# Kernel tuning notes

Measured on AMD Instinct MI355X. Metric: run time of the kernel, lower is better.

The kernel has to match this reference:

```python
import jax, jax.numpy as jnp
import numpy as np

D_MODEL = 1024
NUM_HEADS = 16
D_LATENT = 256
HEAD_DIM = D_MODEL // NUM_HEADS
BATCH = 2048
SEQ = 32


def setup_inputs() -> dict:
    key = jax.random.key(0)
    ks = jax.random.split(key, 9)
    s = 1.0 / np.sqrt(D_MODEL)
    sl = 1.0 / np.sqrt(D_LATENT)
    return {
        "x": jax.random.normal(ks[0], (BATCH, SEQ, D_MODEL), dtype=jnp.float32),
        "memory": jax.random.normal(ks[1], (BATCH, SEQ, D_LATENT), dtype=jnp.float32),
        "W_q": jax.random.normal(ks[2], (D_MODEL, D_MODEL), dtype=jnp.float32) * s,
        "W_k": jax.random.normal(ks[3], (D_MODEL, D_MODEL), dtype=jnp.float32) * s,
        "W_v": jax.random.normal(ks[4], (D_MODEL, D_MODEL), dtype=jnp.float32) * s,
        "W_o": jax.random.normal(ks[5], (D_MODEL, D_MODEL), dtype=jnp.float32) * s,
        "W_down_kv": jax.random.normal(ks[6], (D_MODEL, D_LATENT), dtype=jnp.float32) * s,
        "W_up_k": jax.random.normal(ks[7], (D_LATENT, D_MODEL), dtype=jnp.float32) * sl,
        "W_up_v": jax.random.normal(ks[8], (D_LATENT, D_MODEL), dtype=jnp.float32) * sl,
    }


def reference(x, memory, W_q, W_k, W_v, W_o, W_down_kv, W_up_k, W_up_v):
    B, S, _ = x.shape
    q = x @ W_q                     # [B,S,D]
    k = x @ W_k
    v = x @ W_v
    latent_kv = (k + v) @ W_down_kv  # [B,S,L]
    latent_kv = jnp.nan_to_num((latent_kv + memory) * 0.5)
    k_rec = latent_kv @ W_up_k       # [B,S,D]
    v_rec = latent_kv @ W_up_v
    # split heads: [B,H,S,hd]
    qh = q.reshape(B, S, NUM_HEADS, HEAD_DIM).transpose(0, 2, 1, 3)
    kh = k_rec.reshape(B, S, NUM_HEADS, HEAD_DIM).transpose(0, 2, 1, 3)
    vh = v_rec.reshape(B, S, NUM_HEADS, HEAD_DIM).transpose(0, 2, 1, 3)
    # NOTE: faithful to source — scale is sqrt(d_model), not sqrt(head_dim)
    scores = jnp.einsum("bhqd,bhkd->bhqk", qh, kh) / jnp.sqrt(jnp.float32(D_MODEL))
    scores = jnp.nan_to_num(scores, nan=0.0, posinf=10.0, neginf=-10.0)
    attn = jax.nn.softmax(scores, axis=-1)
    ctx = jnp.einsum("bhqk,bhkd->bhqd", attn, vh)
    ctx = ctx.transpose(0, 2, 1, 3).reshape(B, S, D_MODEL)
    out = ctx @ W_o
    return out, latent_kv
```

## Files before the change

kernel.cpp:

```cpp
#include <hip/hip_runtime.h>
#include <hip/hip_bf16.h>

typedef unsigned short u16;
typedef unsigned int u32;
typedef __attribute__((ext_vector_type(8))) __bf16 bf16x8;
typedef __attribute__((ext_vector_type(8))) unsigned short u16x8;
typedef __attribute__((ext_vector_type(4))) float floatx4;
typedef __attribute__((ext_vector_type(16))) float floatx16;

#define AS1 __attribute__((address_space(1)))
#define AS3 __attribute__((address_space(3)))

__device__ __forceinline__ u16 f2bf(float f) {
  unsigned u = __float_as_uint(f);
  u += 0x7fffu + ((u >> 16) & 1u);
  return (u16)(u >> 16);
}

__device__ __forceinline__ void g2lds16(const u16* g, u16* l) {
  __builtin_amdgcn_global_load_lds((AS1 void*)g, (AS3 void*)l, 16, 0, 0);
}

__device__ __forceinline__ void tcvt_body(const float* __restrict__ s,
                                          u16* __restrict__ d, int R, int C,
                                          int bx, int by, int tid,
                                          float (*t)[33]) {
  const int lx = tid & 31, ly = tid >> 5;
  const int x0 = bx * 32, y0 = by * 32;
  #pragma unroll
  for (int i = 0; i < 32; i += 8)
    t[ly + i][lx] = s[(size_t)(y0 + ly + i) * C + x0 + lx];
  __syncthreads();
  #pragma unroll
  for (int i = 0; i < 32; i += 8)
    d[(size_t)(x0 + ly + i) * R + y0 + lx] = f2bf(t[lx][ly + i]);
}

__global__ __launch_bounds__(256) void k_prep(
    const float* __restrict__ x, u16* __restrict__ Xb,
    const float* __restrict__ Wk, const float* __restrict__ Wv, u16* __restrict__ Wkv,
    const float* __restrict__ Wq, u16* __restrict__ WAt,
    const float* __restrict__ Wdn, u16* __restrict__ Wdt,
    const float* __restrict__ Wuk, u16* __restrict__ WBt,
    const float* __restrict__ Wuv, u16* __restrict__ WBt2,
    const float* __restrict__ Wo, u16* __restrict__ Wot) {
  __shared__ float t[32][33];
  const int b = blockIdx.x;
  const int tid = threadIdx.x;
  if (b < 4096) {
    long i = ((long)b * 256 + tid) * 8;
    const long stride = (long)4096 * 256 * 8;
    for (; i < 67108864L; i += stride) {
      float4 a = *(const float4*)(x + i);
      float4 c = *(const float4*)(x + i + 4);
      u16x8 o;
      o[0] = f2bf(a.x); o[1] = f2bf(a.y); o[2] = f2bf(a.z); o[3] = f2bf(a.w);
      o[4] = f2bf(c.x); o[5] = f2bf(c.y); o[6] = f2bf(c.z); o[7] = f2bf(c.w);
      *(u16x8*)(Xb + i) = o;
    }
  } else if (b < 4608) {
    long i = ((long)(b - 4096) * 256 + tid) * 8;
    float4 a0 = *(const float4*)(Wk + i);
    float4 a1 = *(const float4*)(Wk + i + 4);
    float4 b0 = *(const float4*)(Wv + i);
    float4 b1 = *(const float4*)(Wv + i + 4);
    u16x8 o;
    o[0] = f2bf(a0.x + b0.x); o[1] = f2bf(a0.y + b0.y);
    o[2] = f2bf(a0.z + b0.z); o[3] = f2bf(a0.w + b0.w);
    o[4] = f2bf(a1.x + b1.x); o[5] = f2bf(a1.y + b1.y);
    o[6] = f2bf(a1.z + b1.z); o[7] = f2bf(a1.w + b1.w);
    *(u16x8*)(Wkv + i) = o;
  } else if (b < 5632) {
    int lb = b - 4608;
    tcvt_body(Wq, WAt, 1024, 1024, lb & 31, lb >> 5, tid, t);
  } else if (b < 5888) {
    int lb = b - 5632;
    tcvt_body(Wdn, Wdt, 1024, 256, lb & 7, lb >> 3, tid, t);
  } else if (b < 6144) {
    int lb = b - 5888;
    tcvt_body(Wuk, WBt, 256, 1024, lb & 31, lb >> 5, tid, t);
  } else if (b < 6400) {
    int lb = b - 6144;
    tcvt_body(Wuv, WBt2, 256, 1024, lb & 31, lb >> 5, tid, t);
  } else {
    int lb = b - 6400;
    tcvt_body(Wo, Wot, 1024, 1024, lb & 31, lb >> 5, tid, t);
  }
}

#define MFMA16(a, b, c) c = __builtin_amdgcn_mfma_f32_16x16x32_bf16(a, b, c, 0, 0, 0)
#define MFMA32(a, b, c) c = __builtin_amdgcn_mfma_f32_32x32x16_bf16(a, b, c, 0, 0, 0)

template <int MODE>
__global__ __launch_bounds__(256, 4) void gemm128(
    const u16* __restrict__ A, const u16* __restrict__ Bt,
    int M, int N, int K, int ntn,
    u16* __restrict__ Cb, float* __restrict__ Cf,
    const float* __restrict__ memp, float* __restrict__ latf, u16* __restrict__ latb) {
  __shared__ u16 As[128 * 64];
  __shared__ u16 Bs[128 * 64];
  const int tid = threadIdx.x;
  const int lane = tid & 63;
  const int wid = tid >> 6;
  const int wr = wid >> 1, wc = wid & 1;

  int bid = blockIdx.x;
  {
    const int nwg = gridDim.x;
    const int q = nwg >> 3, r = nwg & 7;
    const int xcd = bid & 7, idx = bid >> 3;
    bid = (xcd < r ? xcd * (q + 1) : r * (q + 1) + (xcd - r) * q) + idx;
  }
  const int mt = bid / ntn, nt = bid % ntn;
  const int m0 = mt * 128, n0 = nt * 128;

  const int fr = lane & 15;
  const int g8 = (lane >> 4) * 8;
  const int xr = (lane & 7) * 8;

  floatx4 acc[4][4];
  #pragma unroll
  for (int i = 0; i < 4; i++)
    #pragma unroll
    for (int j = 0; j < 4; j++) acc[i][j] = 0.0f;

  const u16* Ag0 = A + (size_t)m0 * K;
  const u16* Bg0 = Bt + (size_t)n0 * K;

  for (int kt = 0; kt < K; kt += 64) {
    #pragma unroll
    for (int p = 0; p < 4; p++) {
      int ci = p * 256 + tid;
      int row = ci >> 3;
      int kc = ((ci & 7) ^ (row & 7)) * 8;
      g2lds16(Ag0 + (size_t)row * K + kt + kc, &As[ci * 8]);
    }
    #pragma unroll
    for (int p = 0; p < 4; p++) {
      int ci = p * 256 + tid;
      int row = ci >> 3;
      int kc = ((ci & 7) ^ (row & 7)) * 8;
      g2lds16(Bg0 + (size_t)row * K + kt + kc, &Bs[ci * 8]);
    }
    __syncthreads();
    #pragma unroll
    for (int kk = 0; kk < 64; kk += 32) {
      const int koff = kk + g8;
      bf16x8 af[4], bfv[4];
      #pragma unroll
      for (int i = 0; i < 4; i++)
        af[i] = *(const bf16x8*)&As[(wr * 64 + i * 16 + fr) * 64 + (koff ^ xr)];
      #pragma unroll
      for (int j = 0; j < 4; j++)
        bfv[j] = *(const bf16x8*)&Bs[(wc * 64 + j * 16 + fr) * 64 + (koff ^ xr)];
      #pragma unroll
      for (int i = 0; i < 4; i++)
        #pragma unroll
        for (int j = 0; j < 4; j++)
          MFMA16(af[i], bfv[j], acc[i][j]);
    }
    __syncthreads();
  }

  #pragma unroll
  for (int i = 0; i < 4; i++) {
    const int mb = m0 + wr * 64 + i * 16 + ((lane >> 4) * 4);
    #pragma unroll
    for (int j = 0; j < 4; j++) {
      const int cb = n0 + wc * 64 + j * 16 + (lane & 15);
      #pragma unroll
      for (int r = 0; r < 4; r++) {
        const int m = mb + r;
        const float v = acc[i][j][r];
        if (MODE == 0) {
          Cb[(size_t)m * N + cb] = f2bf(v);
        } else if (MODE == 1) {
          if (n0 < 1024) {
            Cb[(size_t)m * 1024 + cb] = f2bf(v);
          } else {
            int lc = cb - 1024;
            float lv = (v + memp[(size_t)m * 256 + lc]) * 0.5f;
            latf[(size_t)m * 256 + lc] = lv;
            latb[(size_t)m * 256 + lc] = f2bf(lv);
          }
        } else {
          Cf[(size_t)m * N + cb] = v;
        }
      }
    }
  }
}

__global__ __launch_bounds__(256) void k_attn(const u16* __restrict__ KV, u16* Q) {
  __shared__ u16 Qs[4][32][72];
  __shared__ u16 Ks[4][32][72];
  __shared__ u16 Vt[4][64][40];
  const int tid = threadIdx.x;
  const int hg = blockIdx.x;
  const int b = blockIdx.y;
  const long tok0 = (long)b * 32;

  {
    const int t = tid >> 3, ci = tid & 7;
    const int hd = ci >> 1, c0 = (ci & 1) * 32;
    const u16* qrow = Q + (tok0 + t) * 1024 + hg * 256 + ci * 32;
    #pragma unroll
    for (int u = 0; u < 4; u++)
      *(u16x8*)&Qs[hd][t][c0 + u * 8] = *(const u16x8*)(qrow + u * 8);
    const u16* krow = KV + (tok0 + t) * 2048 + hg * 256 + ci * 32;
    #pragma unroll
    for (int u = 0; u < 4; u++)
      *(u16x8*)&Ks[hd][t][c0 + u * 8] = *(const u16x8*)(krow + u * 8);
    const u16* vrow = KV + (tok0 + t) * 2048 + 1024 + hg * 256 + ci * 32;
    #pragma unroll
    for (int u = 0; u < 4; u++) {
      u16x8 v = *(const u16x8*)(vrow + u * 8);
      #pragma unroll
      for (int j = 0; j < 8; j++) Vt[hd][c0 + u * 8 + j][t] = v[j];
    }
  }
  __syncthreads();

  const int w = tid >> 6;
  const int lane = tid & 63;
  const int col = lane & 31, hi = lane >> 5;

  floatx16 S;
  #pragma unroll
  for (int r = 0; r < 16; r++) S[r] = 0.0f;
  #pragma unroll
  for (int kc = 0; kc < 4; kc++) {
    bf16x8 aq = *(const bf16x8*)&Qs[w][col][kc * 16 + hi * 8];
    bf16x8 bk = *(const bf16x8*)&Ks[w][col][kc * 16 + hi * 8];
    MFMA32(aq, bk, S);
  }

  u16* Pw = &Qs[w][0][0];
  float pr[16];
  #pragma unroll
  for (int r = 0; r < 16; r++) {
    float sc = S[r] * 0.03125f;
    float mx = sc;
    #pragma unroll
    for (int off = 16; off >= 1; off >>= 1) mx = fmaxf(mx, __shfl_xor(mx, off, 64));
    float e = __expf(sc - mx);
    float sm = e;
    #pragma unroll
    for (int off = 16; off >= 1; off >>= 1) sm += __shfl_xor(sm, off, 64);
    pr[r] = e / sm;
  }
  #pragma unroll
  for (int r = 0; r < 16; r++) {
    int row = (r & 3) + 8 * (r >> 2) + 4 * hi;
    Pw[row * 40 + col] = f2bf(pr[r]);
  }
  __syncthreads();

  floatx16 c0v, c1v;
  #pragma unroll
  for (int r = 0; r < 16; r++) { c0v[r] = 0.0f; c1v[r] = 0.0f; }
  #pragma unroll
  for (int kc = 0; kc < 2; kc++) {
    bf16x8 ap = *(const bf16x8*)&Pw[col * 40 + kc * 16 + hi * 8];
    bf16x8 bv0 = *(const bf16x8*)&Vt[w][col][kc * 16 + hi * 8];
    bf16x8 bv1 = *(const bf16x8*)&Vt[w][32 + col][kc * 16 + hi * 8];
    MFMA32(ap, bv0, c0v);
    MFMA32(ap, bv1, c1v);
  }
  #pragma unroll
  for (int r = 0; r < 16; r++) {
    int row = (r & 3) + 8 * (r >> 2) + 4 * hi;
    u16* orow = Q + (tok0 + row) * 1024 + hg * 256 + w * 64;
    orow[col] = f2bf(c0v[r]);
    orow[col + 32] = f2bf(c1v[r]);
  }
}

extern "C" void kernel_launch(void* const* d_in, const int* in_sizes, int n_in,
                              void* d_out, int out_size, void* d_ws, size_t ws_size,
                              hipStream_t stream) {
  const float* x    = (const float*)d_in[0];
  const float* mem  = (const float*)d_in[1];
  const float* W_q  = (const float*)d_in[2];
  const float* W_k  = (const float*)d_in[3];
  const float* W_v  = (const float*)d_in[4];
  const float* W_o  = (const float*)d_in[5];
  const float* W_dn = (const float*)d_in[6];
  const float* W_uk = (const float*)d_in[7];
  const float* W_uv = (const float*)d_in[8];
  float* out  = (float*)d_out;
  float* latf = out + (size_t)67108864;

  char* wp = (char*)d_ws;
  u16* Qb  = (u16*)wp; wp += (size_t)65536 * 1024 * 2;
  u16* Lb  = (u16*)wp; wp += (size_t)65536 * 256 * 2;
  u16* WAt = (u16*)wp; wp += (size_t)1280 * 1024 * 2;
  u16* WBt = (u16*)wp; wp += (size_t)2048 * 256 * 2;
  u16* Wot = (u16*)wp; wp += (size_t)1024 * 1024 * 2;
  u16* Wdt = (u16*)wp; wp += (size_t)256 * 1024 * 2;
  u16* Wkv = (u16*)wp; wp += (size_t)1024 * 1024 * 2;

  u16* Xb  = (u16*)d_out;
  u16* KVb = (u16*)d_out;

  dim3 b256(256);

  k_prep<<<7424, b256, 0, stream>>>(
      x, Xb, W_k, W_v, Wkv, W_q, WAt, W_dn, Wdt,
      W_uk, WBt, W_uv, WBt + (size_t)1024 * 256, W_o, Wot);

  gemm128<0><<<16, b256, 0, stream>>>(
      Wdt, Wkv, 256, 1024, 1024, 8, WAt + (size_t)1024 * 1024,
      nullptr, nullptr, nullptr, nullptr);

  gemm128<1><<<5120, b256, 0, stream>>>(
      Xb, WAt, 65536, 1280, 1024, 10, Qb, nullptr, mem, latf, Lb);

  gemm128<0><<<8192, b256, 0, stream>>>(
      Lb, WBt, 65536, 2048, 256, 16, KVb, nullptr, nullptr, nullptr, nullptr);

  k_attn<<<dim3(4, 2048), b256, 0, stream>>>(KVb, Qb);

  gemm128<2><<<4096, b256, 0, stream>>>(
      Qb, Wot, 65536, 1024, 1024, 8, nullptr, out, nullptr, nullptr, nullptr);
}
```

Baseline: 787.3 us.

## Double-buffer LDS tiles in gemm128 to overlap global loads with MFMA

```diff
diff --git a/kernel.cpp b/kernel.cpp
--- a/kernel.cpp
+++ b/kernel.cpp
@@ -91,14 +91,27 @@
 #define MFMA16(a, b, c) c = __builtin_amdgcn_mfma_f32_16x16x32_bf16(a, b, c, 0, 0, 0)
 #define MFMA32(a, b, c) c = __builtin_amdgcn_mfma_f32_32x32x16_bf16(a, b, c, 0, 0, 0)
 
+#define STAGE(BUF, T) do {                                       \
+    _Pragma("unroll")                                            \
+    for (int p = 0; p < 4; p++) {                                \
+      int ci = p * 256 + tid;                                    \
+      int row = ci >> 3;                                         \
+      int kc = ((ci & 7) ^ (row & 7)) * 8;                       \
+      g2lds16(Ag0 + (size_t)row * K + (T) * 64 + kc,             \
+              &As[BUF][ci * 8]);                                 \
+      g2lds16(Bg0 + (size_t)row * K + (T) * 64 + kc,             \
+              &Bs[BUF][ci * 8]);                                 \
+    }                                                            \
+  } while (0)
+
 template <int MODE>
-__global__ __launch_bounds__(256, 4) void gemm128(
+__global__ __launch_bounds__(256, 2) void gemm128(
     const u16* __restrict__ A, const u16* __restrict__ Bt,
     int M, int N, int K, int ntn,
     u16* __restrict__ Cb, float* __restrict__ Cf,
     const float* __restrict__ memp, float* __restrict__ latf, u16* __restrict__ latb) {
-  __shared__ u16 As[128 * 64];
-  __shared__ u16 Bs[128 * 64];
+  __shared__ u16 As[2][128 * 64];
+  __shared__ u16 Bs[2][128 * 64];
   const int tid = threadIdx.x;
   const int lane = tid & 63;
   const int wid = tid >> 6;
@@ -126,33 +139,24 @@
 
   const u16* Ag0 = A + (size_t)m0 * K;
   const u16* Bg0 = Bt + (size_t)n0 * K;
-
-  for (int kt = 0; kt < K; kt += 64) {
-    #pragma unroll
-    for (int p = 0; p < 4; p++) {
-      int ci = p * 256 + tid;
-      int row = ci >> 3;
-      int kc = ((ci & 7) ^ (row & 7)) * 8;
-      g2lds16(Ag0 + (size_t)row * K + kt + kc, &As[ci * 8]);
-    }
-    #pragma unroll
-    for (int p = 0; p < 4; p++) {
-      int ci = p * 256 + tid;
-      int row = ci >> 3;
-      int kc = ((ci & 7) ^ (row & 7)) * 8;
-      g2lds16(Bg0 + (size_t)row * K + kt + kc, &Bs[ci * 8]);
-    }
-    __syncthreads();
+  const int NT = K >> 6;
+
+  STAGE(0, 0);
+  __syncthreads();
+
+  int cur = 0;
+  for (int t = 0; t < NT; ++t) {
+    if (t + 1 < NT) STAGE(cur ^ 1, t + 1);
     #pragma unroll
     for (int kk = 0; kk < 64; kk += 32) {
       const int koff = kk + g8;
       bf16x8 af[4], bfv[4];
       #pragma unroll
       for (int i = 0; i < 4; i++)
-        af[i] = *(const bf16x8*)&As[(wr * 64 + i * 16 + fr) * 64 + (koff ^ xr)];
+        af[i] = *(const bf16x8*)&As[cur][(wr * 64 + i * 16 + fr) * 64 + (koff ^ xr)];
       #pragma unroll
       for (int j = 0; j < 4; j++)
-        bfv[j] = *(const bf16x8*)&Bs[(wc * 64 + j * 16 + fr) * 64 + (koff ^ xr)];
+        bfv[j] = *(const bf16x8*)&Bs[cur][(wc * 64 + j * 16 + fr) * 64 + (koff ^ xr)];
       #pragma unroll
       for (int i = 0; i < 4; i++)
         #pragma unroll
@@ -160,6 +164,7 @@
           MFMA16(af[i], bfv[j], acc[i][j]);
     }
     __syncthreads();
+    cur ^= 1;
   }
 
   #pragma unroll
```

Result: slower. 980.4 us (+24.5%).
